# Performance work log

Measured on AMD Instinct MI355X. Metric: run time of the kernel, lower is better.

## Reference

```python
import jax, jax.numpy as jnp
import numpy as np

B, S, D = 2, 2048, 1024
H, DH = 16, 64  # n_heads, d_head = d_model // n_heads


def setup_inputs() -> dict:
    key = jax.random.key(0)
    ks = jax.random.split(key, 12)
    scale = 1.0 / np.sqrt(D)
    return {
        "queries": jax.random.normal(ks[0], (B, S, D), jnp.float32),
        "keys": jax.random.normal(ks[1], (B, S, D), jnp.float32),
        "values": jax.random.normal(ks[2], (B, S, D), jnp.float32),
        "mask": jax.random.randint(ks[3], (1, 1, S, S), 0, 2, jnp.int32),
        "Wq": jax.random.normal(ks[4], (D, D), jnp.float32) * scale,
        "bq": jnp.zeros((D,), jnp.float32),
        "Wk": jax.random.normal(ks[5], (D, D), jnp.float32) * scale,
        "bk": jnp.zeros((D,), jnp.float32),
        "Wv": jax.random.normal(ks[6], (D, D), jnp.float32) * scale,
        "bv": jnp.zeros((D,), jnp.float32),
        "Wo": jax.random.normal(ks[7], (D, D), jnp.float32) * scale,
        "bo": jnp.zeros((D,), jnp.float32),
    }


def _split_proj(x):
    # (B, ?, H, DH) reshape then permute -> (B, H, ?, DH)
    b = x.shape[0]
    return x.reshape(b, -1, H, DH).transpose(0, 2, 1, 3)


def reference(queries, keys, values, mask, Wq, bq, Wk, bk, Wv, bv, Wo, bo):
    q = queries @ Wq.T + bq
    k = keys @ Wk.T + bk
    v = values @ Wv.T + bv
    # NOTE: original source applies split_proj to queries twice (faithful repro)
    q = _split_proj(_split_proj(q))
    k = _split_proj(k)
    v = _split_proj(v)
    scores = jnp.einsum('bhqd,bhkd->bhqk', q, k) / jnp.sqrt(jnp.float32(DH))
    scores = scores + mask.astype(scores.dtype) * (-1e9)
    attn = jax.nn.softmax(scores, axis=-1)
    out = jnp.einsum('bhqk,bhkd->bhqd', attn, v)  # (B,H,S,DH)
    out = out.transpose(0, 2, 1, 3).reshape(out.shape[0], -1, D)
    return out @ Wo.T + bo
```

## Files before the change

kernel.cpp:

```cpp
#include <hip/hip_runtime.h>
#include <hip/hip_bf16.h>
#include <cstddef>
#include <cstdint>


typedef __attribute__((ext_vector_type(8))) short bf16x8;
typedef __attribute__((ext_vector_type(4))) float f32x4;

__device__ __forceinline__ void gl_lds16(const void* g, void* l) {
    __builtin_amdgcn_global_load_lds(
        (const __attribute__((address_space(1))) void*)g,
        (__attribute__((address_space(3))) void*)l, 16, 0, 0);
}

__global__ __launch_bounds__(256) void convert_all(
    const float* __restrict__ q, const float* __restrict__ k, const float* __restrict__ v,
    const float* __restrict__ wq, const float* __restrict__ wk,
    const float* __restrict__ wv, const float* __restrict__ wo,
    __hip_bfloat16* __restrict__ dq, __hip_bfloat16* __restrict__ dk,
    __hip_bfloat16* __restrict__ dv, __hip_bfloat16* __restrict__ dwq,
    __hip_bfloat16* __restrict__ dwk, __hip_bfloat16* __restrict__ dwv,
    __hip_bfloat16* __restrict__ dwo)
{
    const int bid = blockIdx.x;
    const float* s; __hip_bfloat16* d; int base;
    if      (bid < 2048) { s = q;  d = dq;  base = bid; }
    else if (bid < 4096) { s = k;  d = dk;  base = bid - 2048; }
    else if (bid < 6144) { s = v;  d = dv;  base = bid - 4096; }
    else if (bid < 6656) { s = wq; d = dwq; base = bid - 6144; }
    else if (bid < 7168) { s = wk; d = dwk; base = bid - 6656; }
    else if (bid < 7680) { s = wv; d = dwv; base = bid - 7168; }
    else                 { s = wo; d = dwo; base = bid - 7680; }
    const size_t i = (size_t)base * 256 + threadIdx.x;
    const float4* sp = (const float4*)s + i * 2;
    float4 v0 = sp[0], v1 = sp[1];
    union { __hip_bfloat16 h[8]; int4 qd; } u;
    u.h[0] = __float2bfloat16(v0.x); u.h[1] = __float2bfloat16(v0.y);
    u.h[2] = __float2bfloat16(v0.z); u.h[3] = __float2bfloat16(v0.w);
    u.h[4] = __float2bfloat16(v1.x); u.h[5] = __float2bfloat16(v1.y);
    u.h[6] = __float2bfloat16(v1.z); u.h[7] = __float2bfloat16(v1.w);
    *((int4*)d + i) = u.qd;
}

__global__ __launch_bounds__(256) void packmask(const int* __restrict__ mask,
                                                unsigned long long* __restrict__ mbits)
{
    const int wid  = (blockIdx.x * 256 + threadIdx.x) >> 6;
    const int lane = threadIdx.x & 63;
    const int qr = wid >> 5, w64 = wid & 31;
    const int m = mask[(size_t)qr * 2048 + w64 * 64 + lane];
    const unsigned long long bal = __ballot(m != 0);
    if (lane == 0) mbits[(size_t)qr * 32 + w64] = bal;
}

template <typename OutT>
__device__ __forceinline__ void gemm_body(
    const __hip_bfloat16* __restrict__ A, const __hip_bfloat16* __restrict__ Bm,
    const float* __restrict__ bias, OutT* __restrict__ C,
    int N, int m0, int n0, int brow,
    __hip_bfloat16* As, __hip_bfloat16* Bs)
{
    const int t = threadIdx.x, lane = t & 63, w = t >> 6;
    const int l15 = lane & 15, g = lane >> 4;
    const int wr = w >> 1, wc = w & 1;

    f32x4 acc[4][4] = {};

    for (int k0 = 0; k0 < 1024; k0 += 64) {
        __syncthreads();
        #pragma unroll
        for (int it = 0; it < 4; ++it) {
            const int chunk = it * 256 + w * 64 + lane;
            const int row = chunk >> 3, c = chunk & 7;
            gl_lds16(A  + (size_t)(m0 + row) * 1024 + k0 + c * 8, (char*)As + chunk * 16);
            gl_lds16(Bm + (size_t)(n0 + row) * 1024 + k0 + c * 8, (char*)Bs + chunk * 16);
        }
        __syncthreads();
        #pragma unroll
        for (int kk = 0; kk < 64; kk += 32) {
            bf16x8 af[4], bfr[4];
            #pragma unroll
            for (int i = 0; i < 4; ++i)
                af[i] = *(const bf16x8*)((const char*)As + (wr * 64 + i * 16 + l15) * 128 + kk * 2 + g * 16);
            #pragma unroll
            for (int j = 0; j < 4; ++j)
                bfr[j] = *(const bf16x8*)((const char*)Bs + (wc * 64 + j * 16 + l15) * 128 + kk * 2 + g * 16);
            #pragma unroll
            for (int i = 0; i < 4; ++i)
                #pragma unroll
                for (int j = 0; j < 4; ++j)
                    acc[i][j] = __builtin_amdgcn_mfma_f32_16x16x32_bf16(af[i], bfr[j], acc[i][j], 0, 0, 0);
        }
    }

    #pragma unroll
    for (int i = 0; i < 4; ++i) {
        const int m = m0 + wr * 64 + i * 16 + g * 4;
        #pragma unroll
        for (int j = 0; j < 4; ++j) {
            const int n = n0 + wc * 64 + j * 16 + l15;
            const float bc = brow ? 0.f : bias[n];
            #pragma unroll
            for (int r = 0; r < 4; ++r) {
                const float v = acc[i][j][r] + (brow ? bias[m + r] : bc);
                C[(size_t)(m + r) * N + n] = (OutT)v;
            }
        }
    }
}

__global__ __launch_bounds__(256) void qkv_gemm(
    const __hip_bfloat16* __restrict__ qin, const __hip_bfloat16* __restrict__ kin,
    const __hip_bfloat16* __restrict__ vin,
    const __hip_bfloat16* __restrict__ Wqb, const __hip_bfloat16* __restrict__ Wkb,
    const __hip_bfloat16* __restrict__ Wvb,
    const float* __restrict__ bq, const float* __restrict__ bk, const float* __restrict__ bv,
    __hip_bfloat16* __restrict__ qbuf, __hip_bfloat16* __restrict__ kbuf,
    __hip_bfloat16* __restrict__ vtb)
{
    __shared__ __align__(16) __hip_bfloat16 As[128 * 64];
    __shared__ __align__(16) __hip_bfloat16 Bs[128 * 64];
    const int z = blockIdx.z;
    if (z == 0)
        gemm_body(qin, Wqb, bq, qbuf, 1024, blockIdx.y * 128, blockIdx.x * 128, 0, As, Bs);
    else if (z == 1)
        gemm_body(kin, Wkb, bk, kbuf, 1024, blockIdx.y * 128, blockIdx.x * 128, 0, As, Bs);
    else
        gemm_body(Wvb, vin, bv, vtb, 4096, blockIdx.x * 128, blockIdx.y * 128, 1, As, Bs);
}

__global__ __launch_bounds__(256) void out_gemm(
    const __hip_bfloat16* __restrict__ A, const __hip_bfloat16* __restrict__ Bm,
    const float* __restrict__ bias, float* __restrict__ C)
{
    __shared__ __align__(16) __hip_bfloat16 As[128 * 64];
    __shared__ __align__(16) __hip_bfloat16 Bs[128 * 64];
    gemm_body(A, Bm, bias, C, 1024, blockIdx.y * 128, blockIdx.x * 128, 0, As, Bs);
}

__global__ __launch_bounds__(512) void attn_mfma(
    const __hip_bfloat16* __restrict__ qb,
    const __hip_bfloat16* __restrict__ kb,
    const __hip_bfloat16* __restrict__ vt,
    const unsigned long long* __restrict__ mbits,
    __hip_bfloat16* __restrict__ ctx)
{
    __shared__ __align__(16) __hip_bfloat16 Qs[128 * 64];
    __shared__ __align__(16) __hip_bfloat16 Ks[2][64 * 64];
    __shared__ __align__(16) __hip_bfloat16 Vs[2][64 * 64];
    __shared__ __align__(16) __hip_bfloat16 Pb[8][16 * 64];

    const int t = threadIdx.x, lane = t & 63, w = t >> 6;
    const int l15 = lane & 15, g = lane >> 4;
    const int q0 = blockIdx.x * 128;
    const int bh = blockIdx.y, b = bh >> 4, a = bh & 15;
    const int hq = blockIdx.x;

    constexpr float SC_LOG2E = 0.18033688011112042f;
    constexpr float OFFC     = -17.312340490667561f;
    constexpr float MASKB    = -1.0e9f;

    #pragma unroll
    for (int it = 0; it < 2; ++it) {
        const int c = it * 512 + t;
        const int row = c >> 3, cc = c & 7;
        const int cs = cc ^ (row & 7);
        const int s = row * 16 + a;
        gl_lds16(qb + (size_t)(b * 2048 + s) * 1024 + hq * 64 + cs * 8,
                 (char*)Qs + c * 16);
    }

    auto stage_kv = [&](int buf, int kt) {
        const int c = t;
        const int row = c >> 3, cc = c & 7;
        const int cs = cc ^ (row & 7);
        gl_lds16(kb + (size_t)(b * 2048 + kt * 64 + row) * 1024 + a * 64 + cs * 8,
                 (char*)Ks + buf * 8192 + c * 16);
        gl_lds16(vt + (size_t)(a * 64 + row) * 4096 + b * 2048 + kt * 64 + cs * 8,
                 (char*)Vs + buf * 8192 + c * 16);
    };

    stage_kv(0, 0);
    __syncthreads();

    f32x4 accd[4] = {};
    float l_r = 0.f;
    const int qrow = w * 16 + l15;
    const int qg = q0 + qrow;

    for (int kt = 0; kt < 32; ++kt) {
        const int cur = kt & 1;
        if (kt < 31) stage_kv(cur ^ 1, kt + 1);

        const uint2 mw = *(const uint2*)&mbits[(size_t)qg * 32 + kt];

        f32x4 sf[4] = {};
        #pragma unroll
        for (int half = 0; half < 2; ++half) {
            const int kc = half * 4 + g;
            const bf16x8 qf = *(const bf16x8*)((const char*)Qs + qrow * 128 + ((kc ^ (qrow & 7)) << 4));
            #pragma unroll
            for (int nf = 0; nf < 4; ++nf) {
                const int krow = nf * 16 + l15;
                const bf16x8 kf = *(const bf16x8*)((const char*)Ks + cur * 8192 + krow * 128 + ((kc ^ (krow & 7)) << 4));
                sf[nf] = __builtin_amdgcn_mfma_f32_16x16x32_bf16(kf, qf, sf[nf], 0, 0, 0);
            }
        }

        float psum = 0.f;
        #pragma unroll
        for (int nf = 0; nf < 4; ++nf) {
            const unsigned word = (nf & 2) ? mw.y : mw.x;
            const int bsh = ((nf & 1) << 4) + (g << 2);
            float pr[4];
            #pragma unroll
            for (int r = 0; r < 4; ++r) {
                const bool msk = (word >> (bsh + r)) & 1u;
                pr[r] = exp2f(fmaf(sf[nf][r], SC_LOG2E, msk ? MASKB : OFFC));
            }
            psum += (pr[0] + pr[1]) + (pr[2] + pr[3]);
            __hip_bfloat16 h0 = __float2bfloat16(pr[0]), h1 = __float2bfloat16(pr[1]);
            __hip_bfloat16 h2 = __float2bfloat16(pr[2]), h3 = __float2bfloat16(pr[3]);
            const unsigned w0 = (unsigned)*(unsigned short*)&h0 | ((unsigned)*(unsigned short*)&h1 << 16);
            const unsigned w1 = (unsigned)*(unsigned short*)&h2 | ((unsigned)*(unsigned short*)&h3 << 16);
            char* pb = (char*)Pb + w * 2048 + l15 * 128 +
                       (((2 * nf + (g >> 1)) ^ (l15 & 7)) << 4) + ((g & 1) << 3);
            *(uint2*)pb = make_uint2(w0, w1);
        }
        psum += __shfl_xor(psum, 16);
        psum += __shfl_xor(psum, 32);
        l_r += psum;

        #pragma unroll
        for (int jj = 0; jj < 2; ++jj) {
            const bf16x8 pa = *(const bf16x8*)((const char*)Pb + w * 2048 + l15 * 128 +
                                               (((4 * jj + g) ^ (l15 & 7)) << 4));
            #pragma unroll
            for (int df = 0; df < 4; ++df) {
                const int vrow = df * 16 + l15;
                const bf16x8 vf = *(const bf16x8*)((const char*)Vs + cur * 8192 + vrow * 128 +
                                                   (((4 * jj + g) ^ (vrow & 7)) << 4));
                accd[df] = __builtin_amdgcn_mfma_f32_16x16x32_bf16(pa, vf, accd[df], 0, 0, 0);
            }
        }

        __syncthreads();
    }

    #pragma unroll
    for (int r = 0; r < 4; ++r) {
        const float lq = __shfl(l_r, (g << 2) + r);
        const float inv = 1.0f / lq;
        const int q = q0 + w * 16 + (g << 2) + r;
        #pragma unroll
        for (int df = 0; df < 4; ++df)
            ctx[(size_t)(b * 2048 + q) * 1024 + (a << 6) + df * 16 + l15] =
                __float2bfloat16(accd[df][r] * inv);
    }
}

extern "C" void kernel_launch(void* const* d_in, const int* in_sizes, int n_in,
                              void* d_out, int out_size, void* d_ws, size_t ws_size,
                              hipStream_t stream)
{
    const float* queries = (const float*)d_in[0];
    const float* keys    = (const float*)d_in[1];
    const float* values  = (const float*)d_in[2];
    const int*   mask    = (const int*)  d_in[3];
    const float* Wq = (const float*)d_in[4];
    const float* bq = (const float*)d_in[5];
    const float* Wk = (const float*)d_in[6];
    const float* bk = (const float*)d_in[7];
    const float* Wv = (const float*)d_in[8];
    const float* bv = (const float*)d_in[9];
    const float* Wo = (const float*)d_in[10];
    const float* bo = (const float*)d_in[11];

    const size_t NM = (size_t)4096 * 1024;
    const size_t NW = (size_t)1024 * 1024;
    __hip_bfloat16* p = (__hip_bfloat16*)d_ws;
    __hip_bfloat16* qin = p;  p += NM;
    __hip_bfloat16* kin = p;  p += NM;
    __hip_bfloat16* vin = p;  p += NM;
    __hip_bfloat16* Wqb = p;  p += NW;
    __hip_bfloat16* Wkb = p;  p += NW;
    __hip_bfloat16* Wvb = p;  p += NW;
    __hip_bfloat16* Wob = p;  p += NW;
    __hip_bfloat16* qbuf = p; p += NM;
    __hip_bfloat16* kbuf = p; p += NM;
    __hip_bfloat16* vtb  = p; p += NM;
    unsigned long long* mbits = (unsigned long long*)p;
    __hip_bfloat16* ctxb = qin;

    convert_all<<<dim3(8192), dim3(256), 0, stream>>>(
        queries, keys, values, Wq, Wk, Wv, Wo,
        qin, kin, vin, Wqb, Wkb, Wvb, Wob);
    packmask<<<dim3(16384), dim3(256), 0, stream>>>(mask, mbits);

    qkv_gemm<<<dim3(8, 32, 3), dim3(256), 0, stream>>>(
        qin, kin, vin, Wqb, Wkb, Wvb, bq, bk, bv, qbuf, kbuf, vtb);

    attn_mfma<<<dim3(16, 32), dim3(512), 0, stream>>>(qbuf, kbuf, vtb, mbits, ctxb);

    out_gemm<<<dim3(8, 32), dim3(256), 0, stream>>>(ctxb, Wob, bo, (float*)d_out);
}
```

Measured before the change: 178.8 us.

## Fuse activation bf16 conversion into QKV GEMM and retile attention

Activation fp32-to-bf16 conversion moves out of a separate pass and into the QKV GEMM's tile loads, and only the weights are still pre-converted. This drops a full write and re-read of the three 4096x1024 activation tensors. The attention kernel switches to 256 threads with 32 query rows per wave, keeps Q in registers instead of LDS, and computes row sums with an MFMA against a ones vector instead of shuffles. It also remaps block indices so each XCD handles a group of heads. In exchange, GEMM A loads become synchronous register loads plus LDS stores rather than direct global-to-LDS copies, and attention uses more registers per wave.

Result: slower. 197.3 us (+10.3%).

```diff
diff --git a/kernel.cpp b/kernel.cpp
--- a/kernel.cpp
+++ b/kernel.cpp
@@ -13,33 +13,33 @@
         (__attribute__((address_space(3))) void*)l, 16, 0, 0);
 }
 
-__global__ __launch_bounds__(256) void convert_all(
-    const float* __restrict__ q, const float* __restrict__ k, const float* __restrict__ v,
-    const float* __restrict__ wq, const float* __restrict__ wk,
-    const float* __restrict__ wv, const float* __restrict__ wo,
-    __hip_bfloat16* __restrict__ dq, __hip_bfloat16* __restrict__ dk,
-    __hip_bfloat16* __restrict__ dv, __hip_bfloat16* __restrict__ dwq,
-    __hip_bfloat16* __restrict__ dwk, __hip_bfloat16* __restrict__ dwv,
-    __hip_bfloat16* __restrict__ dwo)
-{
-    const int bid = blockIdx.x;
-    const float* s; __hip_bfloat16* d; int base;
-    if      (bid < 2048) { s = q;  d = dq;  base = bid; }
-    else if (bid < 4096) { s = k;  d = dk;  base = bid - 2048; }
-    else if (bid < 6144) { s = v;  d = dv;  base = bid - 4096; }
-    else if (bid < 6656) { s = wq; d = dwq; base = bid - 6144; }
-    else if (bid < 7168) { s = wk; d = dwk; base = bid - 6656; }
-    else if (bid < 7680) { s = wv; d = dwv; base = bid - 7168; }
-    else                 { s = wo; d = dwo; base = bid - 7680; }
-    const size_t i = (size_t)base * 256 + threadIdx.x;
-    const float4* sp = (const float4*)s + i * 2;
-    float4 v0 = sp[0], v1 = sp[1];
-    union { __hip_bfloat16 h[8]; int4 qd; } u;
+__device__ __forceinline__ int4 cvt8(const float* __restrict__ src) {
+    const float4 v0 = *(const float4*)src, v1 = *(const float4*)(src + 4);
+    union { __hip_bfloat16 h[8]; int4 q; } u;
     u.h[0] = __float2bfloat16(v0.x); u.h[1] = __float2bfloat16(v0.y);
     u.h[2] = __float2bfloat16(v0.z); u.h[3] = __float2bfloat16(v0.w);
     u.h[4] = __float2bfloat16(v1.x); u.h[5] = __float2bfloat16(v1.y);
     u.h[6] = __float2bfloat16(v1.z); u.h[7] = __float2bfloat16(v1.w);
-    *((int4*)d + i) = u.qd;
+    return u.q;
+}
+
+__global__ __launch_bounds__(256) void wconv(
+    const float* __restrict__ wq, const float* __restrict__ wk,
+    const float* __restrict__ wv, const float* __restrict__ wo,
+    __hip_bfloat16* __restrict__ dq, __hip_bfloat16* __restrict__ dk,
+    __hip_bfloat16* __restrict__ dv, __hip_bfloat16* __restrict__ dwo)
+{
+    const int bid = blockIdx.x;
+    const float* s; __hip_bfloat16* d;
+    const int base = bid & 511;
+    switch (bid >> 9) {
+        case 0: s = wq; d = dq;  break;
+        case 1: s = wk; d = dk;  break;
+        case 2: s = wv; d = dv;  break;
+        default: s = wo; d = dwo; break;
+    }
+    const size_t i = (size_t)base * 256 + threadIdx.x;
+    *((int4*)d + i) = cvt8(s + i * 8);
 }
 
 __global__ __launch_bounds__(256) void packmask(const int* __restrict__ mask,
@@ -53,9 +53,9 @@
     if (lane == 0) mbits[(size_t)qr * 32 + w64] = bal;
 }
 
-template <typename OutT>
+template <int AF32, int BF32, typename OutT>
 __device__ __forceinline__ void gemm_body(
-    const __hip_bfloat16* __restrict__ A, const __hip_bfloat16* __restrict__ Bm,
+    const void* __restrict__ A, const void* __restrict__ Bm,
     const float* __restrict__ bias, OutT* __restrict__ C,
     int N, int m0, int n0, int brow,
     __hip_bfloat16* As, __hip_bfloat16* Bs)
@@ -68,12 +68,37 @@
 
     for (int k0 = 0; k0 < 1024; k0 += 64) {
         __syncthreads();
-        #pragma unroll
-        for (int it = 0; it < 4; ++it) {
-            const int chunk = it * 256 + w * 64 + lane;
-            const int row = chunk >> 3, c = chunk & 7;
-            gl_lds16(A  + (size_t)(m0 + row) * 1024 + k0 + c * 8, (char*)As + chunk * 16);
-            gl_lds16(Bm + (size_t)(n0 + row) * 1024 + k0 + c * 8, (char*)Bs + chunk * 16);
+        if (!AF32) {
+            #pragma unroll
+            for (int it = 0; it < 4; ++it) {
+                const int c = it * 256 + t, row = c >> 3, c8 = c & 7;
+                gl_lds16((const __hip_bfloat16*)A + (size_t)(m0 + row) * 1024 + k0 + c8 * 8,
+                         (char*)As + c * 16);
+            }
+        }
+        if (!BF32) {
+            #pragma unroll
+            for (int it = 0; it < 4; ++it) {
+                const int c = it * 256 + t, row = c >> 3, c8 = c & 7;
+                gl_lds16((const __hip_bfloat16*)Bm + (size_t)(n0 + row) * 1024 + k0 + c8 * 8,
+                         (char*)Bs + c * 16);
+            }
+        }
+        if (AF32) {
+            #pragma unroll
+            for (int it = 0; it < 4; ++it) {
+                const int c = it * 256 + t, row = c >> 3, c8 = c & 7;
+                *(int4*)((char*)As + c * 16) =
+                    cvt8((const float*)A + (size_t)(m0 + row) * 1024 + k0 + c8 * 8);
+            }
+        }
+        if (BF32) {
+            #pragma unroll
+            for (int it = 0; it < 4; ++it) {
+                const int c = it * 256 + t, row = c >> 3, c8 = c & 7;
+                *(int4*)((char*)Bs + c * 16) =
+                    cvt8((const float*)Bm + (size_t)(n0 + row) * 1024 + k0 + c8 * 8);
+            }
         }
         __syncthreads();
         #pragma unroll
@@ -110,8 +135,8 @@
 }
 
 __global__ __launch_bounds__(256) void qkv_gemm(
-    const __hip_bfloat16* __restrict__ qin, const __hip_bfloat16* __restrict__ kin,
-    const __hip_bfloat16* __restrict__ vin,
+    const float* __restrict__ qin, const float* __restrict__ kin,
+    const float* __restrict__ vin,
     const __hip_bfloat16* __restrict__ Wqb, const __hip_bfloat16* __restrict__ Wkb,
     const __hip_bfloat16* __restrict__ Wvb,
     const float* __restrict__ bq, const float* __restrict__ bk, const float* __restrict__ bv,
@@ -122,11 +147,14 @@
     __shared__ __align__(16) __hip_bfloat16 Bs[128 * 64];
     const int z = blockIdx.z;
     if (z == 0)
-        gemm_body(qin, Wqb, bq, qbuf, 1024, blockIdx.y * 128, blockIdx.x * 128, 0, As, Bs);
+        gemm_body<1, 0, __hip_bfloat16>(qin, Wqb, bq, qbuf, 1024,
+                                        blockIdx.y * 128, blockIdx.x * 128, 0, As, Bs);
     else if (z == 1)
-        gemm_body(kin, Wkb, bk, kbuf, 1024, blockIdx.y * 128, blockIdx.x * 128, 0, As, Bs);
+        gemm_body<1, 0, __hip_bfloat16>(kin, Wkb, bk, kbuf, 1024,
+                                        blockIdx.y * 128, blockIdx.x * 128, 0, As, Bs);
     else
-        gemm_body(Wvb, vin, bv, vtb, 4096, blockIdx.x * 128, blockIdx.y * 128, 1, As, Bs);
+        gemm_body<0, 1, __hip_bfloat16>(Wvb, vin, bv, vtb, 4096,
+                                        blockIdx.x * 128, blockIdx.y * 128, 1, As, Bs);
 }
 
 __global__ __launch_bounds__(256) void out_gemm(
@@ -135,112 +163,131 @@
 {
     __shared__ __align__(16) __hip_bfloat16 As[128 * 64];
     __shared__ __align__(16) __hip_bfloat16 Bs[128 * 64];
-    gemm_body(A, Bm, bias, C, 1024, blockIdx.y * 128, blockIdx.x * 128, 0, As, Bs);
-}
-
-__global__ __launch_bounds__(512) void attn_mfma(
+    gemm_body<0, 0, float>(A, Bm, bias, C, 1024, blockIdx.y * 128, blockIdx.x * 128, 0, As, Bs);
+}
+
+__global__ __launch_bounds__(256) void attn_mfma(
     const __hip_bfloat16* __restrict__ qb,
     const __hip_bfloat16* __restrict__ kb,
     const __hip_bfloat16* __restrict__ vt,
     const unsigned long long* __restrict__ mbits,
     __hip_bfloat16* __restrict__ ctx)
 {
-    __shared__ __align__(16) __hip_bfloat16 Qs[128 * 64];
     __shared__ __align__(16) __hip_bfloat16 Ks[2][64 * 64];
     __shared__ __align__(16) __hip_bfloat16 Vs[2][64 * 64];
-    __shared__ __align__(16) __hip_bfloat16 Pb[8][16 * 64];
+    __shared__ __align__(16) __hip_bfloat16 Pb[4][32 * 64];
 
     const int t = threadIdx.x, lane = t & 63, w = t >> 6;
     const int l15 = lane & 15, g = lane >> 4;
-    const int q0 = blockIdx.x * 128;
-    const int bh = blockIdx.y, b = bh >> 4, a = bh & 15;
-    const int hq = blockIdx.x;
+
+    const int bid = blockIdx.x;
+    const int xcd = bid & 7, i = bid >> 3;
+    const int bh = (xcd << 2) + (i >> 4), qt = i & 15;
+    const int b = bh >> 4, a = bh & 15;
+    const int q0 = qt * 128;
 
     constexpr float SC_LOG2E = 0.18033688011112042f;
     constexpr float OFFC     = -17.312340490667561f;
     constexpr float MASKB    = -1.0e9f;
 
+    bf16x8 qreg[2][2];
+    int qgl[2];
     #pragma unroll
-    for (int it = 0; it < 2; ++it) {
-        const int c = it * 512 + t;
-        const int row = c >> 3, cc = c & 7;
-        const int cs = cc ^ (row & 7);
-        const int s = row * 16 + a;
-        gl_lds16(qb + (size_t)(b * 2048 + s) * 1024 + hq * 64 + cs * 8,
-                 (char*)Qs + c * 16);
+    for (int u = 0; u < 2; ++u) {
+        const int qg = q0 + w * 32 + u * 16 + l15;
+        qgl[u] = qg;
+        const int hq = qg >> 7;
+        const int srow = (qg & 127) * 16 + a;
+        #pragma unroll
+        for (int half = 0; half < 2; ++half)
+            qreg[u][half] = *(const bf16x8*)&qb[(size_t)(b * 2048 + srow) * 1024 + hq * 64 + (half * 4 + g) * 8];
     }
 
     auto stage_kv = [&](int buf, int kt) {
-        const int c = t;
-        const int row = c >> 3, cc = c & 7;
-        const int cs = cc ^ (row & 7);
-        gl_lds16(kb + (size_t)(b * 2048 + kt * 64 + row) * 1024 + a * 64 + cs * 8,
-                 (char*)Ks + buf * 8192 + c * 16);
-        gl_lds16(vt + (size_t)(a * 64 + row) * 4096 + b * 2048 + kt * 64 + cs * 8,
-                 (char*)Vs + buf * 8192 + c * 16);
+        #pragma unroll
+        for (int it = 0; it < 2; ++it) {
+            const int c = it * 256 + t;
+            const int row = c >> 3, cc = c & 7, cs = cc ^ (row & 7);
+            gl_lds16(kb + (size_t)(b * 2048 + kt * 64 + row) * 1024 + a * 64 + cs * 8,
+                     (char*)Ks + buf * 8192 + c * 16);
+            gl_lds16(vt + (size_t)(a * 64 + row) * 4096 + b * 2048 + kt * 64 + cs * 8,
+                     (char*)Vs + buf * 8192 + c * 16);
+        }
     };
+
+    bf16x8 ones;
+    #pragma unroll
+    for (int e = 0; e < 8; ++e) ones[e] = (short)0x3F80;
+
+    f32x4 accd[2][4] = {};
+    f32x4 accl[2] = {};
 
     stage_kv(0, 0);
     __syncthreads();
-
-    f32x4 accd[4] = {};
-    float l_r = 0.f;
-    const int qrow = w * 16 + l15;
-    const int qg = q0 + qrow;
 
     for (int kt = 0; kt < 32; ++kt) {
         const int cur = kt & 1;
         if (kt < 31) stage_kv(cur ^ 1, kt + 1);
 
-        const uint2 mw = *(const uint2*)&mbits[(size_t)qg * 32 + kt];
-
-        f32x4 sf[4] = {};
+        uint2 mw[2];
+        #pragma unroll
+        for (int u = 0; u < 2; ++u)
+            mw[u] = *(const uint2*)&mbits[(size_t)qgl[u] * 32 + kt];
+
+        f32x4 sf[2][4] = {};
         #pragma unroll
         for (int half = 0; half < 2; ++half) {
             const int kc = half * 4 + g;
-            const bf16x8 qf = *(const bf16x8*)((const char*)Qs + qrow * 128 + ((kc ^ (qrow & 7)) << 4));
             #pragma unroll
             for (int nf = 0; nf < 4; ++nf) {
                 const int krow = nf * 16 + l15;
                 const bf16x8 kf = *(const bf16x8*)((const char*)Ks + cur * 8192 + krow * 128 + ((kc ^ (krow & 7)) << 4));
-                sf[nf] = __builtin_amdgcn_mfma_f32_16x16x32_bf16(kf, qf, sf[nf], 0, 0, 0);
-            }
-        }
-
-        float psum = 0.f;
-        #pragma unroll
-        for (int nf = 0; nf < 4; ++nf) {
-            const unsigned word = (nf & 2) ? mw.y : mw.x;
-            const int bsh = ((nf & 1) << 4) + (g << 2);
-            float pr[4];
-            #pragma unroll
-            for (int r = 0; r < 4; ++r) {
-                const bool msk = (word >> (bsh + r)) & 1u;
-                pr[r] = exp2f(fmaf(sf[nf][r], SC_LOG2E, msk ? MASKB : OFFC));
-            }
-            psum += (pr[0] + pr[1]) + (pr[2] + pr[3]);
-            __hip_bfloat16 h0 = __float2bfloat16(pr[0]), h1 = __float2bfloat16(pr[1]);
-            __hip_bfloat16 h2 = __float2bfloat16(pr[2]), h3 = __float2bfloat16(pr[3]);
-            const unsigned w0 = (unsigned)*(unsigned short*)&h0 | ((unsigned)*(unsigned short*)&h1 << 16);
-            const unsigned w1 = (unsigned)*(unsigned short*)&h2 | ((unsigned)*(unsigned short*)&h3 << 16);
-            char* pb = (char*)Pb + w * 2048 + l15 * 128 +
-                       (((2 * nf + (g >> 1)) ^ (l15 & 7)) << 4) + ((g & 1) << 3);
-            *(uint2*)pb = make_uint2(w0, w1);
-        }
-        psum += __shfl_xor(psum, 16);
-        psum += __shfl_xor(psum, 32);
-        l_r += psum;
+                #pragma unroll
+                for (int u = 0; u < 2; ++u)
+                    sf[u][nf] = __builtin_amdgcn_mfma_f32_16x16x32_bf16(kf, qreg[u][half], sf[u][nf], 0, 0, 0);
+            }
+        }
+
+        #pragma unroll
+        for (int u = 0; u < 2; ++u) {
+            const int prow = u * 16 + l15;
+            char* pbase = (char*)Pb + w * 4096 + prow * 128;
+            #pragma unroll
+            for (int nf = 0; nf < 4; ++nf) {
+                const unsigned word = (nf & 2) ? mw[u].y : mw[u].x;
+                const int bsh = ((nf & 1) << 4) + (g << 2);
+                float pr[4];
+                #pragma unroll
+                for (int r = 0; r < 4; ++r) {
+                    const bool msk = (word >> (bsh + r)) & 1u;
+                    pr[r] = exp2f(fmaf(sf[u][nf][r], SC_LOG2E, msk ? MASKB : OFFC));
+                }
+                __hip_bfloat16 h0 = __float2bfloat16(pr[0]), h1 = __float2bfloat16(pr[1]);
+                __hip_bfloat16 h2 = __float2bfloat16(pr[2]), h3 = __float2bfloat16(pr[3]);
+                const unsigned w0 = (unsigned)*(unsigned short*)&h0 | ((unsigned)*(unsigned short*)&h1 << 16);
+                const unsigned w1 = (unsigned)*(unsigned short*)&h2 | ((unsigned)*(unsigned short*)&h3 << 16);
+                char* pb = pbase + (((2 * nf + (g >> 1)) ^ (prow & 7)) << 4) + ((g & 1) << 3);
+                *(uint2*)pb = make_uint2(w0, w1);
+            }
+        }
 
         #pragma unroll
         for (int jj = 0; jj < 2; ++jj) {
-            const bf16x8 pa = *(const bf16x8*)((const char*)Pb + w * 2048 + l15 * 128 +
-                                               (((4 * jj + g) ^ (l15 & 7)) << 4));
+            const int kc = 4 * jj + g;
+            bf16x8 pa[2];
+            #pragma unroll
+            for (int u = 0; u < 2; ++u) {
+                const int prow = u * 16 + l15;
+                pa[u] = *(const bf16x8*)((const char*)Pb + w * 4096 + prow * 128 + ((kc ^ (prow & 7)) << 4));
+                accl[u] = __builtin_amdgcn_mfma_f32_16x16x32_bf16(pa[u], ones, accl[u], 0, 0, 0);
+            }
             #pragma unroll
             for (int df = 0; df < 4; ++df) {
                 const int vrow = df * 16 + l15;
-                const bf16x8 vf = *(const bf16x8*)((const char*)Vs + cur * 8192 + vrow * 128 +
-                                                   (((4 * jj + g) ^ (vrow & 7)) << 4));
-                accd[df] = __builtin_amdgcn_mfma_f32_16x16x32_bf16(pa, vf, accd[df], 0, 0, 0);
+                const bf16x8 vf = *(const bf16x8*)((const char*)Vs + cur * 8192 + vrow * 128 + ((kc ^ (vrow & 7)) << 4));
+                #pragma unroll
+                for (int u = 0; u < 2; ++u)
+                    accd[u][df] = __builtin_amdgcn_mfma_f32_16x16x32_bf16(pa[u], vf, accd[u][df], 0, 0, 0);
             }
         }
 
@@ -248,14 +295,16 @@
     }
 
     #pragma unroll
-    for (int r = 0; r < 4; ++r) {
-        const float lq = __shfl(l_r, (g << 2) + r);
-        const float inv = 1.0f / lq;
-        const int q = q0 + w * 16 + (g << 2) + r;
-        #pragma unroll
-        for (int df = 0; df < 4; ++df)
-            ctx[(size_t)(b * 2048 + q) * 1024 + (a << 6) + df * 16 + l15] =
-                __float2bfloat16(accd[df][r] * inv);
+    for (int u = 0; u < 2; ++u) {
+        #pragma unroll
+        for (int r = 0; r < 4; ++r) {
+            const float inv = 1.0f / accl[u][r];
+            const int qglob = q0 + w * 32 + u * 16 + (g << 2) + r;
+            #pragma unroll
+            for (int df = 0; df < 4; ++df)
+                ctx[(size_t)(b * 2048 + qglob) * 1024 + (a << 6) + df * 16 + l15] =
+                    __float2bfloat16(accd[u][df][r] * inv);
+        }
     }
 }
 
@@ -279,9 +328,6 @@
     const size_t NM = (size_t)4096 * 1024;
     const size_t NW = (size_t)1024 * 1024;
     __hip_bfloat16* p = (__hip_bfloat16*)d_ws;
-    __hip_bfloat16* qin = p;  p += NM;
-    __hip_bfloat16* kin = p;  p += NM;
-    __hip_bfloat16* vin = p;  p += NM;
     __hip_bfloat16* Wqb = p;  p += NW;
     __hip_bfloat16* Wkb = p;  p += NW;
     __hip_bfloat16* Wvb = p;  p += NW;
@@ -289,18 +335,16 @@
     __hip_bfloat16* qbuf = p; p += NM;
     __hip_bfloat16* kbuf = p; p += NM;
     __hip_bfloat16* vtb  = p; p += NM;
+    __hip_bfloat16* ctxb = p; p += NM;
     unsigned long long* mbits = (unsigned long long*)p;
-    __hip_bfloat16* ctxb = qin;
-
-    convert_all<<<dim3(8192), dim3(256), 0, stream>>>(
-        queries, keys, values, Wq, Wk, Wv, Wo,
-        qin, kin, vin, Wqb, Wkb, Wvb, Wob);
+
+    wconv<<<dim3(2048), dim3(256), 0, stream>>>(Wq, Wk, Wv, Wo, Wqb, Wkb, Wvb, Wob);
     packmask<<<dim3(16384), dim3(256), 0, stream>>>(mask, mbits);
 
     qkv_gemm<<<dim3(8, 32, 3), dim3(256), 0, stream>>>(
-        qin, kin, vin, Wqb, Wkb, Wvb, bq, bk, bv, qbuf, kbuf, vtb);
-
-    attn_mfma<<<dim3(16, 32), dim3(512), 0, stream>>>(qbuf, kbuf, vtb, mbits, ctxb);
+        queries, keys, values, Wqb, Wkb, Wvb, bq, bk, bv, qbuf, kbuf, vtb);
+
+    attn_mfma<<<dim3(512), dim3(256), 0, stream>>>(qbuf, kbuf, vtb, mbits, ctxb);
 
     out_gemm<<<dim3(8, 32), dim3(256), 0, stream>>>(ctxb, Wob, bo, (float*)d_out);
 }
```
